# Kernel tuning notes

Measured on AMD Instinct MI355X. Metric: run time of the kernel, lower is better.

Reference implementation:

```python
import jax, jax.numpy as jnp
import numpy as np

D_MODEL = 1024
N_HEADS = 16
D_K = D_MODEL // N_HEADS
D_FF = 4096
THETA = 10000.0
B, S = 2, 2048
EPS = 1e-5


def _trunc_normal(key, shape, fan_in, fan_out):
    std = np.sqrt(2.0 / (fan_in + fan_out))
    return std * jax.random.truncated_normal(key, -3.0, 3.0, shape, dtype=jnp.float32)


def setup_inputs() -> dict:
    key = jax.random.key(0)
    ks = jax.random.split(key, 9)
    x = jax.random.normal(ks[0], (B, S, D_MODEL), dtype=jnp.float32)
    wq = _trunc_normal(ks[1], (D_MODEL, D_MODEL), D_MODEL, D_MODEL)
    wk = _trunc_normal(ks[2], (D_MODEL, D_MODEL), D_MODEL, D_MODEL)
    wv = _trunc_normal(ks[3], (D_MODEL, D_MODEL), D_MODEL, D_MODEL)
    wo = _trunc_normal(ks[4], (D_MODEL, D_MODEL), D_MODEL, D_MODEL)
    w1 = _trunc_normal(ks[5], (D_FF, D_MODEL), D_MODEL, D_FF)
    w2 = _trunc_normal(ks[6], (D_MODEL, D_FF), D_FF, D_MODEL)
    w3 = _trunc_normal(ks[7], (D_FF, D_MODEL), D_MODEL, D_FF)
    g1 = jnp.ones((D_MODEL,), dtype=jnp.float32)
    g2 = jnp.ones((D_MODEL,), dtype=jnp.float32)
    return {"x": x, "wq": wq, "wk": wk, "wv": wv, "wo": wo,
            "w1": w1, "w2": w2, "w3": w3, "g1": g1, "g2": g2}


def _rmsnorm(x, gain):
    xf = x.astype(jnp.float32)
    rms = jnp.sqrt(jnp.mean(xf * xf, axis=-1, keepdims=True) + EPS)
    return (xf / rms * gain).astype(x.dtype)


def _rope(x):
    # x: [B, H, S, D_K]; block-diag 2x2 rotations on consecutive pairs
    s, d = x.shape[-2], x.shape[-1]
    pos = jnp.arange(s, dtype=jnp.float32)  # [S]
    k = jnp.arange(d // 2, dtype=jnp.float32)
    ang = pos[:, None] / (THETA ** (2.0 * k / d))[None, :]  # [S, d/2]
    cos, sin = jnp.cos(ang), jnp.sin(ang)
    xp = x.reshape(*x.shape[:-1], d // 2, 2)
    x0, x1 = xp[..., 0], xp[..., 1]
    r0 = cos * x0 - sin * x1
    r1 = sin * x0 + cos * x1
    return jnp.stack([r0, r1], axis=-1).reshape(x.shape)


def reference(x, wq, wk, wv, wo, w1, w2, w3, g1, g2):
    # --- attention sublayer ---
    h = _rmsnorm(x, g1)
    q = h @ wq.T
    k = h @ wk.T
    v = h @ wv.T
    def split_heads(t):
        b, s, _ = t.shape
        return t.reshape(b, s, N_HEADS, D_K).transpose(0, 2, 1, 3)  # [B,H,S,Dk]
    q, k, v = split_heads(q), split_heads(k), split_heads(v)
    q, k = _rope(q), _rope(k)
    scores = jnp.einsum('bhqd,bhkd->bhqk', q, k) / jnp.sqrt(jnp.float32(D_K))
    s = x.shape[-2]
    causal = jnp.tril(jnp.ones((s, s), dtype=bool))
    scores = jnp.where(causal, scores, -jnp.inf)
    attn = jax.nn.softmax(scores, axis=-1)
    o = jnp.einsum('bhqk,bhkd->bhqd', attn, v)
    o = o.transpose(0, 2, 1, 3).reshape(x.shape[0], s, D_MODEL)
    x = x + o @ wo.T
    # --- SwiGLU FFN sublayer ---
    h2 = _rmsnorm(x, g2)
    a = h2 @ w1.T
    gate = a * jax.nn.sigmoid(a)
    ff = (gate * (h2 @ w3.T)) @ w2.T
    return x + ff
```

## Files before the change

kernel.cpp:

```cpp
#include <hip/hip_runtime.h>
#include <hip/hip_bf16.h>
#include <cstddef>
#include <cstdint>

#define D_MODEL 1024
#define N_HEADS 16
#define D_K     64
#define D_FF    4096
#define BATCH   2
#define SEQ     2048
#define TOKENS  (BATCH * SEQ)
#define EPS     1e-5f

typedef __attribute__((ext_vector_type(8))) short short8;
typedef __attribute__((ext_vector_type(4))) float f32x4;

#define MFMA_BF16 __builtin_amdgcn_mfma_f32_16x16x32_bf16

static __device__ __forceinline__ short f2bf(float f) {
    __hip_bfloat16 h = __float2bfloat16(f);
    short s;
    __builtin_memcpy(&s, &h, 2);
    return s;
}
static __device__ __forceinline__ float bf2f(short s) {
    __hip_bfloat16 h;
    __builtin_memcpy(&h, &s, 2);
    return __bfloat162float(h);
}

static __device__ __forceinline__ void async_ld16(const short* g, short* l) {
    __builtin_amdgcn_global_load_lds(
        (const __attribute__((address_space(1))) void*)g,
        (__attribute__((address_space(3))) void*)l,
        16, 0, 0);
}

__global__ __launch_bounds__(256) void cvt_weights(
    const float* wq, const float* wk, const float* wv, const float* wo,
    const float* w1, const float* w3, const float* w2, short* dst)
{
    const size_t M1 = 1 << 20;
    size_t e = ((size_t)blockIdx.x * 256 + threadIdx.x) * 4;
    const float* src;
    size_t off;
    if (e < M1)            { src = wq; off = e; }
    else if (e < 2 * M1)   { src = wk; off = e - M1; }
    else if (e < 3 * M1)   { src = wv; off = e - 2 * M1; }
    else if (e < 4 * M1)   { src = wo; off = e - 3 * M1; }
    else if (e < 12 * M1) {
        size_t r = (e - 4 * M1) >> 10;
        size_t col = e & 1023;
        size_t p = r >> 5, half = (r >> 4) & 1, idx = r & 15;
        src = half ? w3 : w1;
        off = (p * 16 + idx) * 1024 + col;
    }
    else                   { src = w2; off = e - 12 * M1; }
    float4 v = *reinterpret_cast<const float4*>(src + off);
    short4 o;
    o.x = f2bf(v.x); o.y = f2bf(v.y); o.z = f2bf(v.z); o.w = f2bf(v.w);
    *reinterpret_cast<short4*>(dst + e) = o;
}

__global__ __launch_bounds__(256) void rmsnorm_kernel(
    const float* __restrict__ x, const float* __restrict__ g,
    __hip_bfloat16* __restrict__ out)
{
    int row = blockIdx.x;
    int tid = threadIdx.x;
    int lane = tid & 63, wave = tid >> 6;
    const float4* xv = reinterpret_cast<const float4*>(x + (size_t)row * D_MODEL);
    float4 v = xv[tid];
    float ss = v.x * v.x + v.y * v.y + v.z * v.z + v.w * v.w;
#pragma unroll
    for (int m = 1; m < 64; m <<= 1) ss += __shfl_xor(ss, m, 64);
    __shared__ float red[4];
    if (lane == 0) red[wave] = ss;
    __syncthreads();
    float tot = red[0] + red[1] + red[2] + red[3];
    float inv = 1.0f / sqrtf(tot * (1.0f / D_MODEL) + EPS);
    float4 gv = reinterpret_cast<const float4*>(g)[tid];
    size_t base = (size_t)row * D_MODEL + (size_t)tid * 4;
    out[base + 0] = __float2bfloat16(v.x * inv * gv.x);
    out[base + 1] = __float2bfloat16(v.y * inv * gv.y);
    out[base + 2] = __float2bfloat16(v.z * inv * gv.z);
    out[base + 3] = __float2bfloat16(v.w * inv * gv.w);
}

__global__ __launch_bounds__(256) void resid_norm_kernel(
    const float* __restrict__ x, const float* __restrict__ P,
    const float* __restrict__ g, float* __restrict__ out,
    __hip_bfloat16* __restrict__ h)
{
    int row = blockIdx.x;
    int tid = threadIdx.x;
    int lane = tid & 63, wave = tid >> 6;
    size_t base = (size_t)row * D_MODEL + (size_t)tid * 4;
    float4 v  = *reinterpret_cast<const float4*>(x + base);
    float4 p0 = *reinterpret_cast<const float4*>(P + base);
    float4 p1 = *reinterpret_cast<const float4*>(P + (size_t)TOKENS * D_MODEL + base);
    v.x += p0.x + p1.x; v.y += p0.y + p1.y;
    v.z += p0.z + p1.z; v.w += p0.w + p1.w;
    *reinterpret_cast<float4*>(out + base) = v;
    float ss = v.x * v.x + v.y * v.y + v.z * v.z + v.w * v.w;
#pragma unroll
    for (int m = 1; m < 64; m <<= 1) ss += __shfl_xor(ss, m, 64);
    __shared__ float red[4];
    if (lane == 0) red[wave] = ss;
    __syncthreads();
    float tot = red[0] + red[1] + red[2] + red[3];
    float inv = 1.0f / sqrtf(tot * (1.0f / D_MODEL) + EPS);
    float4 gv = reinterpret_cast<const float4*>(g)[tid];
    h[base + 0] = __float2bfloat16(v.x * inv * gv.x);
    h[base + 1] = __float2bfloat16(v.y * inv * gv.y);
    h[base + 2] = __float2bfloat16(v.z * inv * gv.z);
    h[base + 3] = __float2bfloat16(v.w * inv * gv.w);
}

__global__ __launch_bounds__(256) void final_add_kernel(
    float* __restrict__ out, const float* __restrict__ Q)
{
    size_t base = ((size_t)blockIdx.x * 256 + threadIdx.x) * 4;
    float4 v  = *reinterpret_cast<const float4*>(out + base);
    float4 q0 = *reinterpret_cast<const float4*>(Q + base);
    float4 q1 = *reinterpret_cast<const float4*>(Q + (size_t)TOKENS * D_MODEL + base);
    v.x += q0.x + q1.x; v.y += q0.y + q1.y;
    v.z += q0.z + q1.z; v.w += q0.w + q1.w;
    *reinterpret_cast<float4*>(out + base) = v;
}

template<int EPI>
__global__ __launch_bounds__(256) void gemm_bt(
    const short* __restrict__ A, const short* __restrict__ W,
    void* __restrict__ Cout, int K, int lda, int ldc)
{
    __shared__ short Alds[128 * 64];
    __shared__ short Blds[128 * 64];

    const int lane = threadIdx.x & 63;
    const int wv = threadIdx.x >> 6;
    const int quad = lane >> 4, l16 = lane & 15;
    const int wm = wv & 1, wn = wv >> 1;
    const int rowblk = blockIdx.y * 128;
    const int colblk = blockIdx.x * 128;

    const int srow = lane >> 2;
    const int sseg = ((lane & 3) - (lane >> 3)) & 3;
    const short* sA0 = A + (size_t)(rowblk + wv * 16 + srow) * lda + sseg * 8;
    const short* sA1 = A + (size_t)(rowblk + (wv + 4) * 16 + srow) * lda + sseg * 8;
    const short* sB0 = W + (size_t)(colblk + wv * 16 + srow) * (size_t)K + sseg * 8;
    const short* sB1 = W + (size_t)(colblk + (wv + 4) * 16 + srow) * (size_t)K + sseg * 8;
    short* lA0 = &Alds[wv * 512];
    short* lA1 = &Alds[(wv + 4) * 512];
    short* lB0 = &Blds[wv * 512];
    short* lB1 = &Blds[(wv + 4) * 512];

    int aoff[4], boff[4];
#pragma unroll
    for (int i = 0; i < 4; ++i) {
        int tr = wm * 64 + i * 16 + l16;
        aoff[i] = tr * 32 + ((quad + (tr >> 1)) & 3) * 8;
        int tc = wn * 64 + i * 16 + l16;
        boff[i] = tc * 32 + ((quad + (tc >> 1)) & 3) * 8;
    }

    f32x4 acc[4][4];
#pragma unroll
    for (int i = 0; i < 4; ++i)
#pragma unroll
        for (int j = 0; j < 4; ++j)
            acc[i][j] = (f32x4){0.f, 0.f, 0.f, 0.f};

    for (int kk = 0; kk < K; kk += 64) {
        if (kk) __syncthreads();
        async_ld16(sA0 + kk, lA0);
        async_ld16(sA1 + kk, lA1);
        async_ld16(sB0 + kk, lB0);
        async_ld16(sB1 + kk, lB1);
        async_ld16(sA0 + kk + 32, lA0 + 4096);
        async_ld16(sA1 + kk + 32, lA1 + 4096);
        async_ld16(sB0 + kk + 32, lB0 + 4096);
        async_ld16(sB1 + kk + 32, lB1 + 4096);
        __syncthreads();
#pragma unroll
        for (int hf = 0; hf < 2; ++hf) {
            short8 af[4], bf[4];
#pragma unroll
            for (int i = 0; i < 4; ++i)
                af[i] = *reinterpret_cast<const short8*>(&Alds[hf * 4096 + aoff[i]]);
#pragma unroll
            for (int j = 0; j < 4; ++j)
                bf[j] = *reinterpret_cast<const short8*>(&Blds[hf * 4096 + boff[j]]);
#pragma unroll
            for (int i = 0; i < 4; ++i)
#pragma unroll
                for (int j = 0; j < 4; ++j)
                    acc[i][j] = MFMA_BF16(af[i], bf[j], acc[i][j], 0, 0, 0);
        }
    }

    if (EPI == 2) {
#pragma unroll
        for (int i = 0; i < 4; ++i) {
#pragma unroll
            for (int jp = 0; jp < 2; ++jp) {
#pragma unroll
                for (int r = 0; r < 4; ++r) {
                    int row = rowblk + wm * 64 + i * 16 + quad * 4 + r;
                    int col = blockIdx.x * 64 + wn * 32 + jp * 16 + l16;
                    float a = acc[i][2 * jp][r];
                    float b3 = acc[i][2 * jp + 1][r];
                    float gv = a / (1.f + __expf(-a)) * b3;
                    reinterpret_cast<__hip_bfloat16*>(Cout)[(size_t)row * ldc + col] =
                        __float2bfloat16(gv);
                }
            }
        }
    } else {
#pragma unroll
        for (int i = 0; i < 4; ++i) {
#pragma unroll
            for (int j = 0; j < 4; ++j) {
#pragma unroll
                for (int r = 0; r < 4; ++r) {
                    int row = rowblk + wm * 64 + i * 16 + quad * 4 + r;
                    int col = colblk + wn * 64 + j * 16 + l16;
                    size_t idx = (size_t)row * ldc + col;
                    if (EPI == 3)
                        reinterpret_cast<__hip_bfloat16*>(Cout)[idx] =
                            __float2bfloat16(acc[i][j][r]);
                    else
                        reinterpret_cast<float*>(Cout)[idx] = acc[i][j][r];
                }
            }
        }
    }
}

template<int SPLIT>
__global__ __launch_bounds__(256) void gemm_bt_sk(
    const short* __restrict__ A, const short* __restrict__ W,
    float* __restrict__ P, int K, int lda, int ldc)
{
    __shared__ short Alds[128 * 64];
    __shared__ short Blds[128 * 64];

    const int Kc = K / SPLIT;
    const int kbase = blockIdx.z * Kc;
    float* Cout = P + (size_t)blockIdx.z * TOKENS * ldc;

    const int lane = threadIdx.x & 63;
    const int wv = threadIdx.x >> 6;
    const int quad = lane >> 4, l16 = lane & 15;
    const int wm = wv & 1, wn = wv >> 1;
    const int rowblk = blockIdx.y * 128;
    const int colblk = blockIdx.x * 128;

    const int srow = lane >> 2;
    const int sseg = ((lane & 3) - (lane >> 3)) & 3;
    const short* sA0 = A + (size_t)(rowblk + wv * 16 + srow) * lda + kbase + sseg * 8;
    const short* sA1 = A + (size_t)(rowblk + (wv + 4) * 16 + srow) * lda + kbase + sseg * 8;
    const short* sB0 = W + (size_t)(colblk + wv * 16 + srow) * (size_t)K + kbase + sseg * 8;
    const short* sB1 = W + (size_t)(colblk + (wv + 4) * 16 + srow) * (size_t)K + kbase + sseg * 8;
    short* lA0 = &Alds[wv * 512];
    short* lA1 = &Alds[(wv + 4) * 512];
    short* lB0 = &Blds[wv * 512];
    short* lB1 = &Blds[(wv + 4) * 512];

    int aoff[4], boff[4];
#pragma unroll
    for (int i = 0; i < 4; ++i) {
        int tr = wm * 64 + i * 16 + l16;
        aoff[i] = tr * 32 + ((quad + (tr >> 1)) & 3) * 8;
        int tc = wn * 64 + i * 16 + l16;
        boff[i] = tc * 32 + ((quad + (tc >> 1)) & 3) * 8;
    }

    f32x4 acc[4][4];
#pragma unroll
    for (int i = 0; i < 4; ++i)
#pragma unroll
        for (int j = 0; j < 4; ++j)
            acc[i][j] = (f32x4){0.f, 0.f, 0.f, 0.f};

    for (int kk = 0; kk < Kc; kk += 64) {
        if (kk) __syncthreads();
        async_ld16(sA0 + kk, lA0);
        async_ld16(sA1 + kk, lA1);
        async_ld16(sB0 + kk, lB0);
        async_ld16(sB1 + kk, lB1);
        async_ld16(sA0 + kk + 32, lA0 + 4096);
        async_ld16(sA1 + kk + 32, lA1 + 4096);
        async_ld16(sB0 + kk + 32, lB0 + 4096);
        async_ld16(sB1 + kk + 32, lB1 + 4096);
        __syncthreads();
#pragma unroll
        for (int hf = 0; hf < 2; ++hf) {
            short8 af[4], bf[4];
#pragma unroll
            for (int i = 0; i < 4; ++i)
                af[i] = *reinterpret_cast<const short8*>(&Alds[hf * 4096 + aoff[i]]);
#pragma unroll
            for (int j = 0; j < 4; ++j)
                bf[j] = *reinterpret_cast<const short8*>(&Blds[hf * 4096 + boff[j]]);
#pragma unroll
            for (int i = 0; i < 4; ++i)
#pragma unroll
                for (int j = 0; j < 4; ++j)
                    acc[i][j] = MFMA_BF16(af[i], bf[j], acc[i][j], 0, 0, 0);
        }
    }

#pragma unroll
    for (int i = 0; i < 4; ++i) {
#pragma unroll
        for (int j = 0; j < 4; ++j) {
#pragma unroll
            for (int r = 0; r < 4; ++r) {
                int row = rowblk + wm * 64 + i * 16 + quad * 4 + r;
                int col = colblk + wn * 64 + j * 16 + l16;
                Cout[(size_t)row * ldc + col] = acc[i][j][r];
            }
        }
    }
}

__global__ __launch_bounds__(256) void rope_kernel(
    const short* __restrict__ qk,
    __hip_bfloat16* __restrict__ qb, __hip_bfloat16* __restrict__ kb)
{
    int idx = blockIdx.x * 256 + threadIdx.x;
    int p = idx & 31;
    int h = (idx >> 5) & 15;
    int tok = idx >> 9;
    int s = tok & (SEQ - 1);
    int b = tok >> 11;
    float invf = exp2f((float)p * -(0.03125f * 13.287712379549449f));
    float ang = (float)s * invf;
    float c, sn;
    sincosf(ang, &sn, &c);
    size_t base = (size_t)tok * 3072 + h * 64 + 2 * p;
    float q0 = bf2f(qk[base]),           q1 = bf2f(qk[base + 1]);
    float k0 = bf2f(qk[base + D_MODEL]), k1 = bf2f(qk[base + D_MODEL + 1]);
    float cq = c * 0.125f, sq = sn * 0.125f;
    size_t ob = ((size_t)(b * N_HEADS + h) * SEQ + s) * D_K + 2 * p;
    qb[ob]     = __float2bfloat16(cq * q0 - sq * q1);
    qb[ob + 1] = __float2bfloat16(sq * q0 + cq * q1);
    kb[ob]     = __float2bfloat16(c * k0 - sn * k1);
    kb[ob + 1] = __float2bfloat16(sn * k0 + c * k1);
}

__global__ __launch_bounds__(256) void vtrans_kernel(
    const short* __restrict__ qk, __hip_bfloat16* __restrict__ vt)
{
    __shared__ float tile[64 * 65];
    const int bh = blockIdx.y;
    const int s0 = blockIdx.x * 64;
    const int t = threadIdx.x;
    const int r = t >> 4, c4 = (t & 15) * 4;
    const short* src = qk + ((size_t)(bh >> 4) * SEQ + s0) * 3072 + 2048 + (bh & 15) * 64;
#pragma unroll
    for (int p = 0; p < 4; ++p) {
        int s = p * 16 + r;
        short4 v = *reinterpret_cast<const short4*>(src + (size_t)s * 3072 + c4);
        tile[s * 65 + c4 + 0] = bf2f(v.x);
        tile[s * 65 + c4 + 1] = bf2f(v.y);
        tile[s * 65 + c4 + 2] = bf2f(v.z);
        tile[s * 65 + c4 + 3] = bf2f(v.w);
    }
    __syncthreads();
    const int d = t >> 2, sg = (t & 3) * 16;
    __hip_bfloat16* dst = vt + ((size_t)bh * 64 + d) * SEQ + s0 + sg;
    short8 o0, o1;
#pragma unroll
    for (int i = 0; i < 8; ++i) o0[i] = f2bf(tile[(sg + i) * 65 + d]);
#pragma unroll
    for (int i = 0; i < 8; ++i) o1[i] = f2bf(tile[(sg + 8 + i) * 65 + d]);
    *reinterpret_cast<short8*>(dst) = o0;
    *reinterpret_cast<short8*>(dst + 8) = o1;
}

__global__ __launch_bounds__(256) void attn_kernel(
    const __hip_bfloat16* __restrict__ qbp, const __hip_bfloat16* __restrict__ kbp,
    const __hip_bfloat16* __restrict__ vtp, __hip_bfloat16* __restrict__ o)
{
    const int wave = threadIdx.x >> 6;
    const int lane = threadIdx.x & 63;
    const int quad = lane >> 4, l16 = lane & 15;
    const int bh = blockIdx.y;
    const int qt = blockIdx.x;
    const int q0 = qt * 128 + wave * 32;

    const short* Q  = reinterpret_cast<const short*>(qbp) + ((size_t)bh * SEQ + q0) * D_K;
    const short* Kg = reinterpret_cast<const short*>(kbp) + (size_t)bh * SEQ * D_K;
    const short* Vg = reinterpret_cast<const short*>(vtp) + (size_t)bh * D_K * SEQ;

    short8 qfr[2][2];
#pragma unroll
    for (int f = 0; f < 2; ++f) {
        qfr[f][0] = *reinterpret_cast<const short8*>(Q + (size_t)(f * 16 + l16) * D_K + quad * 8);
        qfr[f][1] = *reinterpret_cast<const short8*>(Q + (size_t)(f * 16 + l16) * D_K + 32 + quad * 8);
    }

    f32x4 oacc[2][4];
    f32x4 lacc[2];
#pragma unroll
    for (int f = 0; f < 2; ++f) {
        lacc[f] = (f32x4){0.f, 0.f, 0.f, 0.f};
#pragma unroll
        for (int g = 0; g < 4; ++g) oacc[f][g] = (f32x4){0.f, 0.f, 0.f, 0.f};
    }

    short8 ones;
#pragma unroll
    for (int i = 0; i < 8; ++i) ones[i] = (short)0x3F80;

    __shared__ short Kt[64 * 64];
    __shared__ short Vl[64 * 64];
    __shared__ short plds[4][32 * 72];
    short* myP = &plds[wave][0];

    const int srl = lane >> 3;
    const int sp  = lane & 7;

    const int ntile = 2 * qt + 2;
    for (int tile = 0; tile < ntile; ++tile) {
        const int kb0 = tile * 64;
        if (tile) __syncthreads();
#pragma unroll
        for (int j = 0; j < 2; ++j) {
            int r0 = j * 32 + wave * 8;
            int t  = r0 + srl;
            int sl = (sp - t) & 7;
            async_ld16(Kg + (size_t)(kb0 + t) * D_K + sl * 8, &Kt[r0 * 64]);
            async_ld16(Vg + (size_t)t * SEQ + kb0 + sl * 8, &Vl[r0 * 64]);
        }
        __syncthreads();

        f32x4 sf[2][4];
#pragma unroll
        for (int kg = 0; kg < 4; ++kg) {
            int row = kg * 16 + l16;
            const short* kr = &Kt[row * 64];
            short8 kf0 = *reinterpret_cast<const short8*>(&kr[((quad + row) & 7) * 8]);
            short8 kf1 = *reinterpret_cast<const short8*>(&kr[((quad + 4 + row) & 7) * 8]);
#pragma unroll
            for (int f = 0; f < 2; ++f) {
                f32x4 z = (f32x4){0.f, 0.f, 0.f, 0.f};
                z = MFMA_BF16(qfr[f][0], kf0, z, 0, 0, 0);
                z = MFMA_BF16(qfr[f][1], kf1, z, 0, 0, 0);
                sf[f][kg] = z;
            }
        }
#pragma unroll
        for (int f = 0; f < 2; ++f) {
            const int qlo = q0 + f * 16;
#pragma unroll
            for (int kg = 0; kg < 4; ++kg) {
                const int keylo = kb0 + kg * 16;
                const bool needmask = keylo >= qlo;
                const int key = keylo + l16;
#pragma unroll
                for (int r = 0; r < 4; ++r) {
                    float p = __expf(sf[f][kg][r]);
                    if (needmask) {
                        int qrow = qlo + quad * 4 + r;
                        p = (key > qrow) ? 0.f : p;
                    }
                    myP[(f * 16 + quad * 4 + r) * 72 + kg * 16 + l16] = f2bf(p);
                }
            }
        }
        asm volatile("s_waitcnt lgkmcnt(0)" ::: "memory");
        short8 pf[2][2];
#pragma unroll
        for (int f = 0; f < 2; ++f) {
#pragma unroll
            for (int hh = 0; hh < 2; ++hh) {
                pf[f][hh] = *reinterpret_cast<const short8*>(
                    &myP[(f * 16 + l16) * 72 + (hh * 4 + quad) * 8]);
                lacc[f] = MFMA_BF16(pf[f][hh], ones, lacc[f], 0, 0, 0);
            }
        }
#pragma unroll
        for (int g = 0; g < 4; ++g) {
            int rd = g * 16 + l16;
            const short* vr = &Vl[rd * 64];
            short8 vf0 = *reinterpret_cast<const short8*>(&vr[((quad + rd) & 7) * 8]);
            short8 vf1 = *reinterpret_cast<const short8*>(&vr[((quad + 4 + rd) & 7) * 8]);
#pragma unroll
            for (int f = 0; f < 2; ++f) {
                oacc[f][g] = MFMA_BF16(pf[f][0], vf0, oacc[f][g], 0, 0, 0);
                oacc[f][g] = MFMA_BF16(pf[f][1], vf1, oacc[f][g], 0, 0, 0);
            }
        }
    }

    const int b = bh >> 4, h = bh & 15;
#pragma unroll
    for (int f = 0; f < 2; ++f) {
#pragma unroll
        for (int g = 0; g < 4; ++g) {
#pragma unroll
            for (int r = 0; r < 4; ++r) {
                int qrow = q0 + f * 16 + quad * 4 + r;
                float v = oacc[f][g][r] / lacc[f][r];
                o[(size_t)(b * SEQ + qrow) * D_MODEL + h * 64 + g * 16 + l16] =
                    __float2bfloat16(v);
            }
        }
    }
}

extern "C" void kernel_launch(void* const* d_in, const int* in_sizes, int n_in,
                              void* d_out, int out_size, void* d_ws, size_t ws_size,
                              hipStream_t stream)
{
    const float* x  = (const float*)d_in[0];
    const float* wq = (const float*)d_in[1];
    const float* wk = (const float*)d_in[2];
    const float* wv = (const float*)d_in[3];
    const float* wo = (const float*)d_in[4];
    const float* w1 = (const float*)d_in[5];
    const float* w2 = (const float*)d_in[6];
    const float* w3 = (const float*)d_in[7];
    const float* g1 = (const float*)d_in[8];
    const float* g2 = (const float*)d_in[9];
    float* out = (float*)d_out;

    char* ws = (char*)d_ws;
    const size_t OFF_WTS  = 0;
    const size_t OFF_H    = 33554432;
    const size_t OFF_QKV  = 41943040;
    const size_t OFF_QB   = 92274688;
    const size_t OFF_KB   = 100663296;
    const size_t OFF_VT   = 109051904;
    const size_t OFF_O    = 117440512;
    const size_t OFF_P    = OFF_QKV;
    const size_t OFF_GATE = OFF_QKV;
    const size_t OFF_Q2   = OFF_QB;

    short* wts  = (short*)(ws + OFF_WTS);
    short* wqkvb = wts;
    short* wob  = wts + (size_t)3 * (1 << 20);
    short* w13b = wts + (size_t)4 * (1 << 20);
    short* w2b  = wts + (size_t)12 * (1 << 20);
    __hip_bfloat16* h  = (__hip_bfloat16*)(ws + OFF_H);
    short* qkvb = (short*)(ws + OFF_QKV);
    __hip_bfloat16* qb = (__hip_bfloat16*)(ws + OFF_QB);
    __hip_bfloat16* kb = (__hip_bfloat16*)(ws + OFF_KB);
    __hip_bfloat16* vt = (__hip_bfloat16*)(ws + OFF_VT);
    __hip_bfloat16* ob = (__hip_bfloat16*)(ws + OFF_O);
    float* Pwo  = (float*)(ws + OFF_P);
    __hip_bfloat16* gate = (__hip_bfloat16*)(ws + OFF_GATE);
    float* Qw2  = (float*)(ws + OFF_Q2);

    cvt_weights<<<16384, 256, 0, stream>>>(wq, wk, wv, wo, w1, w3, w2, wts);
    rmsnorm_kernel<<<TOKENS, 256, 0, stream>>>(x, g1, h);
    gemm_bt<3><<<dim3(3072 / 128, TOKENS / 128), 256, 0, stream>>>(
        (const short*)h, wqkvb, qkvb, D_MODEL, D_MODEL, 3072);
    rope_kernel<<<8192, 256, 0, stream>>>(qkvb, qb, kb);
    vtrans_kernel<<<dim3(SEQ / 64, BATCH * N_HEADS), 256, 0, stream>>>(qkvb, vt);
    attn_kernel<<<dim3(SEQ / 128, BATCH * N_HEADS), 256, 0, stream>>>(qb, kb, vt, ob);
    gemm_bt_sk<2><<<dim3(D_MODEL / 128, TOKENS / 128, 2), 256, 0, stream>>>(
        (const short*)ob, wob, Pwo, D_MODEL, D_MODEL, D_MODEL);
    resid_norm_kernel<<<TOKENS, 256, 0, stream>>>(x, Pwo, g2, out, h);
    gemm_bt<2><<<dim3(8192 / 128, TOKENS / 128), 256, 0, stream>>>(
        (const short*)h, w13b, gate, D_MODEL, D_MODEL, D_FF);
    gemm_bt_sk<2><<<dim3(D_MODEL / 128, TOKENS / 128, 2), 256, 0, stream>>>(
        (const short*)gate, w2b, Qw2, D_FF, D_FF, D_MODEL);
    final_add_kernel<<<TOKENS * D_MODEL / 1024, 256, 0, stream>>>(out, Qw2);
    (void)in_sizes; (void)n_in; (void)out_size; (void)ws_size;
}
```

Before: 399.3 us.

## Merge prep kernels, store split-K partials in bf16, skip masked attention tiles

Weight conversion and the first RMSNorm now run in one launch, and RoPE and the V transpose run in another, which removes two kernel launches. The split-K GEMM partials are written as bf16 instead of fp32, halving their write and read traffic in the residual and final-add kernels, at some cost in accuracy. The attention kernel skips the score and PV computation for key tiles that lie entirely above the causal diagonal of each wave's query rows, though it still loads those tiles and synchronises on them.

```diff
diff --git a/kernel.cpp b/kernel.cpp
--- a/kernel.cpp
+++ b/kernel.cpp
@@ -36,59 +36,57 @@
         16, 0, 0);
 }
 
-__global__ __launch_bounds__(256) void cvt_weights(
+__global__ __launch_bounds__(256) void prep_kernel(
     const float* wq, const float* wk, const float* wv, const float* wo,
-    const float* w1, const float* w3, const float* w2, short* dst)
-{
-    const size_t M1 = 1 << 20;
-    size_t e = ((size_t)blockIdx.x * 256 + threadIdx.x) * 4;
-    const float* src;
-    size_t off;
-    if (e < M1)            { src = wq; off = e; }
-    else if (e < 2 * M1)   { src = wk; off = e - M1; }
-    else if (e < 3 * M1)   { src = wv; off = e - 2 * M1; }
-    else if (e < 4 * M1)   { src = wo; off = e - 3 * M1; }
-    else if (e < 12 * M1) {
-        size_t r = (e - 4 * M1) >> 10;
-        size_t col = e & 1023;
-        size_t p = r >> 5, half = (r >> 4) & 1, idx = r & 15;
-        src = half ? w3 : w1;
-        off = (p * 16 + idx) * 1024 + col;
-    }
-    else                   { src = w2; off = e - 12 * M1; }
-    float4 v = *reinterpret_cast<const float4*>(src + off);
-    short4 o;
-    o.x = f2bf(v.x); o.y = f2bf(v.y); o.z = f2bf(v.z); o.w = f2bf(v.w);
-    *reinterpret_cast<short4*>(dst + e) = o;
-}
-
-__global__ __launch_bounds__(256) void rmsnorm_kernel(
-    const float* __restrict__ x, const float* __restrict__ g,
-    __hip_bfloat16* __restrict__ out)
-{
-    int row = blockIdx.x;
-    int tid = threadIdx.x;
-    int lane = tid & 63, wave = tid >> 6;
-    const float4* xv = reinterpret_cast<const float4*>(x + (size_t)row * D_MODEL);
-    float4 v = xv[tid];
-    float ss = v.x * v.x + v.y * v.y + v.z * v.z + v.w * v.w;
-#pragma unroll
-    for (int m = 1; m < 64; m <<= 1) ss += __shfl_xor(ss, m, 64);
-    __shared__ float red[4];
-    if (lane == 0) red[wave] = ss;
-    __syncthreads();
-    float tot = red[0] + red[1] + red[2] + red[3];
-    float inv = 1.0f / sqrtf(tot * (1.0f / D_MODEL) + EPS);
-    float4 gv = reinterpret_cast<const float4*>(g)[tid];
-    size_t base = (size_t)row * D_MODEL + (size_t)tid * 4;
-    out[base + 0] = __float2bfloat16(v.x * inv * gv.x);
-    out[base + 1] = __float2bfloat16(v.y * inv * gv.y);
-    out[base + 2] = __float2bfloat16(v.z * inv * gv.z);
-    out[base + 3] = __float2bfloat16(v.w * inv * gv.w);
+    const float* w1, const float* w3, const float* w2, short* dst,
+    const float* x, const float* g1, __hip_bfloat16* h)
+{
+    if (blockIdx.x < 16384) {
+        const size_t M1 = 1 << 20;
+        size_t e = ((size_t)blockIdx.x * 256 + threadIdx.x) * 4;
+        const float* src;
+        size_t off;
+        if (e < M1)            { src = wq; off = e; }
+        else if (e < 2 * M1)   { src = wk; off = e - M1; }
+        else if (e < 3 * M1)   { src = wv; off = e - 2 * M1; }
+        else if (e < 4 * M1)   { src = wo; off = e - 3 * M1; }
+        else if (e < 12 * M1) {
+            size_t r = (e - 4 * M1) >> 10;
+            size_t col = e & 1023;
+            size_t p = r >> 5, half = (r >> 4) & 1, idx = r & 15;
+            src = half ? w3 : w1;
+            off = (p * 16 + idx) * 1024 + col;
+        }
+        else                   { src = w2; off = e - 12 * M1; }
+        float4 v = *reinterpret_cast<const float4*>(src + off);
+        short4 o;
+        o.x = f2bf(v.x); o.y = f2bf(v.y); o.z = f2bf(v.z); o.w = f2bf(v.w);
+        *reinterpret_cast<short4*>(dst + e) = o;
+    } else {
+        int row = blockIdx.x - 16384;
+        int tid = threadIdx.x;
+        int lane = tid & 63, wave = tid >> 6;
+        const float4* xv = reinterpret_cast<const float4*>(x + (size_t)row * D_MODEL);
+        float4 v = xv[tid];
+        float ss = v.x * v.x + v.y * v.y + v.z * v.z + v.w * v.w;
+#pragma unroll
+        for (int m = 1; m < 64; m <<= 1) ss += __shfl_xor(ss, m, 64);
+        __shared__ float red[4];
+        if (lane == 0) red[wave] = ss;
+        __syncthreads();
+        float tot = red[0] + red[1] + red[2] + red[3];
+        float inv = 1.0f / sqrtf(tot * (1.0f / D_MODEL) + EPS);
+        float4 gv = reinterpret_cast<const float4*>(g1)[tid];
+        size_t base = (size_t)row * D_MODEL + (size_t)tid * 4;
+        h[base + 0] = __float2bfloat16(v.x * inv * gv.x);
+        h[base + 1] = __float2bfloat16(v.y * inv * gv.y);
+        h[base + 2] = __float2bfloat16(v.z * inv * gv.z);
+        h[base + 3] = __float2bfloat16(v.w * inv * gv.w);
+    }
 }
 
 __global__ __launch_bounds__(256) void resid_norm_kernel(
-    const float* __restrict__ x, const float* __restrict__ P,
+    const float* __restrict__ x, const short* __restrict__ P,
     const float* __restrict__ g, float* __restrict__ out,
     __hip_bfloat16* __restrict__ h)
 {
@@ -96,11 +94,11 @@
     int tid = threadIdx.x;
     int lane = tid & 63, wave = tid >> 6;
     size_t base = (size_t)row * D_MODEL + (size_t)tid * 4;
-    float4 v  = *reinterpret_cast<const float4*>(x + base);
-    float4 p0 = *reinterpret_cast<const float4*>(P + base);
-    float4 p1 = *reinterpret_cast<const float4*>(P + (size_t)TOKENS * D_MODEL + base);
-    v.x += p0.x + p1.x; v.y += p0.y + p1.y;
-    v.z += p0.z + p1.z; v.w += p0.w + p1.w;
+    float4 v = *reinterpret_cast<const float4*>(x + base);
+    short4 p0 = *reinterpret_cast<const short4*>(P + base);
+    short4 p1 = *reinterpret_cast<const short4*>(P + (size_t)TOKENS * D_MODEL + base);
+    v.x += bf2f(p0.x) + bf2f(p1.x); v.y += bf2f(p0.y) + bf2f(p1.y);
+    v.z += bf2f(p0.z) + bf2f(p1.z); v.w += bf2f(p0.w) + bf2f(p1.w);
     *reinterpret_cast<float4*>(out + base) = v;
     float ss = v.x * v.x + v.y * v.y + v.z * v.z + v.w * v.w;
 #pragma unroll
@@ -118,14 +116,14 @@
 }
 
 __global__ __launch_bounds__(256) void final_add_kernel(
-    float* __restrict__ out, const float* __restrict__ Q)
+    float* __restrict__ out, const short* __restrict__ Q)
 {
     size_t base = ((size_t)blockIdx.x * 256 + threadIdx.x) * 4;
-    float4 v  = *reinterpret_cast<const float4*>(out + base);
-    float4 q0 = *reinterpret_cast<const float4*>(Q + base);
-    float4 q1 = *reinterpret_cast<const float4*>(Q + (size_t)TOKENS * D_MODEL + base);
-    v.x += q0.x + q1.x; v.y += q0.y + q1.y;
-    v.z += q0.z + q1.z; v.w += q0.w + q1.w;
+    float4 v = *reinterpret_cast<const float4*>(out + base);
+    short4 q0 = *reinterpret_cast<const short4*>(Q + base);
+    short4 q1 = *reinterpret_cast<const short4*>(Q + (size_t)TOKENS * D_MODEL + base);
+    v.x += bf2f(q0.x) + bf2f(q1.x); v.y += bf2f(q0.y) + bf2f(q1.y);
+    v.z += bf2f(q0.z) + bf2f(q1.z); v.w += bf2f(q0.w) + bf2f(q1.w);
     *reinterpret_cast<float4*>(out + base) = v;
 }
 
@@ -240,14 +238,14 @@
 template<int SPLIT>
 __global__ __launch_bounds__(256) void gemm_bt_sk(
     const short* __restrict__ A, const short* __restrict__ W,
-    float* __restrict__ P, int K, int lda, int ldc)
+    short* __restrict__ P, int K, int lda, int ldc)
 {
     __shared__ short Alds[128 * 64];
     __shared__ short Blds[128 * 64];
 
     const int Kc = K / SPLIT;
     const int kbase = blockIdx.z * Kc;
-    float* Cout = P + (size_t)blockIdx.z * TOKENS * ldc;
+    short* Cout = P + (size_t)blockIdx.z * TOKENS * ldc;
 
     const int lane = threadIdx.x & 63;
     const int wv = threadIdx.x >> 6;
@@ -319,65 +317,65 @@
             for (int r = 0; r < 4; ++r) {
                 int row = rowblk + wm * 64 + i * 16 + quad * 4 + r;
                 int col = colblk + wn * 64 + j * 16 + l16;
-                Cout[(size_t)row * ldc + col] = acc[i][j][r];
-            }
-        }
-    }
-}
-
-__global__ __launch_bounds__(256) void rope_kernel(
+                Cout[(size_t)row * ldc + col] = f2bf(acc[i][j][r]);
+            }
+        }
+    }
+}
+
+__global__ __launch_bounds__(256) void qkv_post_kernel(
     const short* __restrict__ qk,
-    __hip_bfloat16* __restrict__ qb, __hip_bfloat16* __restrict__ kb)
-{
-    int idx = blockIdx.x * 256 + threadIdx.x;
-    int p = idx & 31;
-    int h = (idx >> 5) & 15;
-    int tok = idx >> 9;
-    int s = tok & (SEQ - 1);
-    int b = tok >> 11;
-    float invf = exp2f((float)p * -(0.03125f * 13.287712379549449f));
-    float ang = (float)s * invf;
-    float c, sn;
-    sincosf(ang, &sn, &c);
-    size_t base = (size_t)tok * 3072 + h * 64 + 2 * p;
-    float q0 = bf2f(qk[base]),           q1 = bf2f(qk[base + 1]);
-    float k0 = bf2f(qk[base + D_MODEL]), k1 = bf2f(qk[base + D_MODEL + 1]);
-    float cq = c * 0.125f, sq = sn * 0.125f;
-    size_t ob = ((size_t)(b * N_HEADS + h) * SEQ + s) * D_K + 2 * p;
-    qb[ob]     = __float2bfloat16(cq * q0 - sq * q1);
-    qb[ob + 1] = __float2bfloat16(sq * q0 + cq * q1);
-    kb[ob]     = __float2bfloat16(c * k0 - sn * k1);
-    kb[ob + 1] = __float2bfloat16(sn * k0 + c * k1);
-}
-
-__global__ __launch_bounds__(256) void vtrans_kernel(
-    const short* __restrict__ qk, __hip_bfloat16* __restrict__ vt)
+    __hip_bfloat16* __restrict__ qb, __hip_bfloat16* __restrict__ kb,
+    __hip_bfloat16* __restrict__ vt)
 {
     __shared__ float tile[64 * 65];
-    const int bh = blockIdx.y;
-    const int s0 = blockIdx.x * 64;
-    const int t = threadIdx.x;
-    const int r = t >> 4, c4 = (t & 15) * 4;
-    const short* src = qk + ((size_t)(bh >> 4) * SEQ + s0) * 3072 + 2048 + (bh & 15) * 64;
-#pragma unroll
-    for (int p = 0; p < 4; ++p) {
-        int s = p * 16 + r;
-        short4 v = *reinterpret_cast<const short4*>(src + (size_t)s * 3072 + c4);
-        tile[s * 65 + c4 + 0] = bf2f(v.x);
-        tile[s * 65 + c4 + 1] = bf2f(v.y);
-        tile[s * 65 + c4 + 2] = bf2f(v.z);
-        tile[s * 65 + c4 + 3] = bf2f(v.w);
-    }
-    __syncthreads();
-    const int d = t >> 2, sg = (t & 3) * 16;
-    __hip_bfloat16* dst = vt + ((size_t)bh * 64 + d) * SEQ + s0 + sg;
-    short8 o0, o1;
-#pragma unroll
-    for (int i = 0; i < 8; ++i) o0[i] = f2bf(tile[(sg + i) * 65 + d]);
-#pragma unroll
-    for (int i = 0; i < 8; ++i) o1[i] = f2bf(tile[(sg + 8 + i) * 65 + d]);
-    *reinterpret_cast<short8*>(dst) = o0;
-    *reinterpret_cast<short8*>(dst + 8) = o1;
+    if (blockIdx.x < 8192) {
+        int idx = blockIdx.x * 256 + threadIdx.x;
+        int p = idx & 31;
+        int h = (idx >> 5) & 15;
+        int tok = idx >> 9;
+        int s = tok & (SEQ - 1);
+        int b = tok >> 11;
+        float invf = exp2f((float)p * -(0.03125f * 13.287712379549449f));
+        float ang = (float)s * invf;
+        float c, sn;
+        sincosf(ang, &sn, &c);
+        size_t base = (size_t)tok * 3072 + h * 64 + 2 * p;
+        float q0 = bf2f(qk[base]),           q1 = bf2f(qk[base + 1]);
+        float k0 = bf2f(qk[base + D_MODEL]), k1 = bf2f(qk[base + D_MODEL + 1]);
+        float cq = c * 0.125f, sq = sn * 0.125f;
+        size_t ob = ((size_t)(b * N_HEADS + h) * SEQ + s) * D_K + 2 * p;
+        qb[ob]     = __float2bfloat16(cq * q0 - sq * q1);
+        qb[ob + 1] = __float2bfloat16(sq * q0 + cq * q1);
+        kb[ob]     = __float2bfloat16(c * k0 - sn * k1);
+        kb[ob + 1] = __float2bfloat16(sn * k0 + c * k1);
+    } else {
+        int bid = blockIdx.x - 8192;
+        const int bh = bid >> 5;
+        const int s0 = (bid & 31) * 64;
+        const int t = threadIdx.x;
+        const int r = t >> 4, c4 = (t & 15) * 4;
+        const short* src = qk + ((size_t)(bh >> 4) * SEQ + s0) * 3072 + 2048 + (bh & 15) * 64;
+#pragma unroll
+        for (int p = 0; p < 4; ++p) {
+            int s = p * 16 + r;
+            short4 v = *reinterpret_cast<const short4*>(src + (size_t)s * 3072 + c4);
+            tile[s * 65 + c4 + 0] = bf2f(v.x);
+            tile[s * 65 + c4 + 1] = bf2f(v.y);
+            tile[s * 65 + c4 + 2] = bf2f(v.z);
+            tile[s * 65 + c4 + 3] = bf2f(v.w);
+        }
+        __syncthreads();
+        const int d = t >> 2, sg = (t & 3) * 16;
+        __hip_bfloat16* dst = vt + ((size_t)bh * 64 + d) * SEQ + s0 + sg;
+        short8 o0, o1;
+#pragma unroll
+        for (int i = 0; i < 8; ++i) o0[i] = f2bf(tile[(sg + i) * 65 + d]);
+#pragma unroll
+        for (int i = 0; i < 8; ++i) o1[i] = f2bf(tile[(sg + 8 + i) * 65 + d]);
+        *reinterpret_cast<short8*>(dst) = o0;
+        *reinterpret_cast<short8*>(dst + 8) = o1;
+    }
 }
 
 __global__ __launch_bounds__(256) void attn_kernel(
@@ -390,6 +388,7 @@
     const int bh = blockIdx.y;
     const int qt = blockIdx.x;
     const int q0 = qt * 128 + wave * 32;
+    const int qmax = q0 + 31;
 
     const short* Q  = reinterpret_cast<const short*>(qbp) + ((size_t)bh * SEQ + q0) * D_K;
     const short* Kg = reinterpret_cast<const short*>(kbp) + (size_t)bh * SEQ * D_K;
@@ -437,61 +436,63 @@
         }
         __syncthreads();
 
-        f32x4 sf[2][4];
-#pragma unroll
-        for (int kg = 0; kg < 4; ++kg) {
-            int row = kg * 16 + l16;
-            const short* kr = &Kt[row * 64];
-            short8 kf0 = *reinterpret_cast<const short8*>(&kr[((quad + row) & 7) * 8]);
-            short8 kf1 = *reinterpret_cast<const short8*>(&kr[((quad + 4 + row) & 7) * 8]);
+        if (kb0 <= qmax) {
+            f32x4 sf[2][4];
+#pragma unroll
+            for (int kg = 0; kg < 4; ++kg) {
+                int row = kg * 16 + l16;
+                const short* kr = &Kt[row * 64];
+                short8 kf0 = *reinterpret_cast<const short8*>(&kr[((quad + row) & 7) * 8]);
+                short8 kf1 = *reinterpret_cast<const short8*>(&kr[((quad + 4 + row) & 7) * 8]);
+#pragma unroll
+                for (int f = 0; f < 2; ++f) {
+                    f32x4 z = (f32x4){0.f, 0.f, 0.f, 0.f};
+                    z = MFMA_BF16(qfr[f][0], kf0, z, 0, 0, 0);
+                    z = MFMA_BF16(qfr[f][1], kf1, z, 0, 0, 0);
+                    sf[f][kg] = z;
+                }
+            }
 #pragma unroll
             for (int f = 0; f < 2; ++f) {
-                f32x4 z = (f32x4){0.f, 0.f, 0.f, 0.f};
-                z = MFMA_BF16(qfr[f][0], kf0, z, 0, 0, 0);
-                z = MFMA_BF16(qfr[f][1], kf1, z, 0, 0, 0);
-                sf[f][kg] = z;
-            }
-        }
-#pragma unroll
-        for (int f = 0; f < 2; ++f) {
-            const int qlo = q0 + f * 16;
-#pragma unroll
-            for (int kg = 0; kg < 4; ++kg) {
-                const int keylo = kb0 + kg * 16;
-                const bool needmask = keylo >= qlo;
-                const int key = keylo + l16;
-#pragma unroll
-                for (int r = 0; r < 4; ++r) {
-                    float p = __expf(sf[f][kg][r]);
-                    if (needmask) {
-                        int qrow = qlo + quad * 4 + r;
-                        p = (key > qrow) ? 0.f : p;
+                const int qlo = q0 + f * 16;
+#pragma unroll
+                for (int kg = 0; kg < 4; ++kg) {
+                    const int keylo = kb0 + kg * 16;
+                    const bool needmask = keylo >= qlo;
+                    const int key = keylo + l16;
+#pragma unroll
+                    for (int r = 0; r < 4; ++r) {
+                        float p = __expf(sf[f][kg][r]);
+                        if (needmask) {
+                            int qrow = qlo + quad * 4 + r;
+                            p = (key > qrow) ? 0.f : p;
+                        }
+                        myP[(f * 16 + quad * 4 + r) * 72 + kg * 16 + l16] = f2bf(p);
                     }
-                    myP[(f * 16 + quad * 4 + r) * 72 + kg * 16 + l16] = f2bf(p);
                 }
             }
-        }
-        asm volatile("s_waitcnt lgkmcnt(0)" ::: "memory");
-        short8 pf[2][2];
-#pragma unroll
-        for (int f = 0; f < 2; ++f) {
-#pragma unroll
-            for (int hh = 0; hh < 2; ++hh) {
-                pf[f][hh] = *reinterpret_cast<const short8*>(
-                    &myP[(f * 16 + l16) * 72 + (hh * 4 + quad) * 8]);
-                lacc[f] = MFMA_BF16(pf[f][hh], ones, lacc[f], 0, 0, 0);
-            }
-        }
-#pragma unroll
-        for (int g = 0; g < 4; ++g) {
-            int rd = g * 16 + l16;
-            const short* vr = &Vl[rd * 64];
-            short8 vf0 = *reinterpret_cast<const short8*>(&vr[((quad + rd) & 7) * 8]);
-            short8 vf1 = *reinterpret_cast<const short8*>(&vr[((quad + 4 + rd) & 7) * 8]);
+            asm volatile("s_waitcnt lgkmcnt(0)" ::: "memory");
+            short8 pf[2][2];
 #pragma unroll
             for (int f = 0; f < 2; ++f) {
-                oacc[f][g] = MFMA_BF16(pf[f][0], vf0, oacc[f][g], 0, 0, 0);
-                oacc[f][g] = MFMA_BF16(pf[f][1], vf1, oacc[f][g], 0, 0, 0);
+#pragma unroll
+                for (int hh = 0; hh < 2; ++hh) {
+                    pf[f][hh] = *reinterpret_cast<const short8*>(
+                        &myP[(f * 16 + l16) * 72 + (hh * 4 + quad) * 8]);
+                    lacc[f] = MFMA_BF16(pf[f][hh], ones, lacc[f], 0, 0, 0);
+                }
+            }
+#pragma unroll
+            for (int g = 0; g < 4; ++g) {
+                int rd = g * 16 + l16;
+                const short* vr = &Vl[rd * 64];
+                short8 vf0 = *reinterpret_cast<const short8*>(&vr[((quad + rd) & 7) * 8]);
+                short8 vf1 = *reinterpret_cast<const short8*>(&vr[((quad + 4 + rd) & 7) * 8]);
+#pragma unroll
+                for (int f = 0; f < 2; ++f) {
+                    oacc[f][g] = MFMA_BF16(pf[f][0], vf0, oacc[f][g], 0, 0, 0);
+                    oacc[f][g] = MFMA_BF16(pf[f][1], vf1, oacc[f][g], 0, 0, 0);
+                }
             }
         }
     }
@@ -551,16 +552,14 @@
     __hip_bfloat16* kb = (__hip_bfloat16*)(ws + OFF_KB);
     __hip_bfloat16* vt = (__hip_bfloat16*)(ws + OFF_VT);
     __hip_bfloat16* ob = (__hip_bfloat16*)(ws + OFF_O);
-    float* Pwo  = (float*)(ws + OFF_P);
+    short* Pwo  = (short*)(ws + OFF_P);
     __hip_bfloat16* gate = (__hip_bfloat16*)(ws + OFF_GATE);
-    float* Qw2  = (float*)(ws + OFF_Q2);
-
-    cvt_weights<<<16384, 256, 0, stream>>>(wq, wk, wv, wo, w1, w3, w2, wts);
-    rmsnorm_kernel<<<TOKENS, 256, 0, stream>>>(x, g1, h);
+    short* Qw2  = (short*)(ws + OFF_Q2);
+
+    prep_kernel<<<20480, 256, 0, stream>>>(wq, wk, wv, wo, w1, w3, w2, wts, x, g1, h);
     gemm_bt<3><<<dim3(3072 / 128, TOKENS / 128), 256, 0, stream>>>(
         (const short*)h, wqkvb, qkvb, D_MODEL, D_MODEL, 3072);
-    rope_kernel<<<8192, 256, 0, stream>>>(qkvb, qb, kb);
-    vtrans_kernel<<<dim3(SEQ / 64, BATCH * N_HEADS), 256, 0, stream>>>(qkvb, vt);
+    qkv_post_kernel<<<9216, 256, 0, stream>>>(qkvb, qb, kb, vt);
     attn_kernel<<<dim3(SEQ / 128, BATCH * N_HEADS), 256, 0, stream>>>(qb, kb, vt, ob);
     gemm_bt_sk<2><<<dim3(D_MODEL / 128, TOKENS / 128, 2), 256, 0, stream>>>(
         (const short*)ob, wob, Pwo, D_MODEL, D_MODEL, D_MODEL);
```

Measured after the change: 383.7 us. -3.9%, faster.
